# Kernel optimization log

Measured on AMD Instinct MI355X. Metric: run time of the kernel, lower is better.

Reference implementation:

```python
import jax, jax.numpy as jnp
import numpy as np

B, T, H = 2, 2048, 1024
DFF = 4 * H        # dense_mlp hidden width
E = 8              # num_experts_temp
TOP_K = 2


def setup_inputs() -> dict:
    key = jax.random.key(0)
    ks = jax.random.split(key, 6)
    s_h = 1.0 / np.sqrt(H)
    s_f = 1.0 / np.sqrt(DFF)
    return {
        "hidden_states": jax.random.normal(ks[0], (B, T, H), dtype=jnp.float32),
        "router_w": jax.random.normal(ks[1], (E, H), dtype=jnp.float32) * s_h,
        "w1": jax.random.normal(ks[2], (E, H, DFF), dtype=jnp.float32) * s_h,
        "b1": jnp.zeros((E, DFF), dtype=jnp.float32),
        "w2": jax.random.normal(ks[3], (E, DFF, H), dtype=jnp.float32) * s_f,
        "b2": jnp.zeros((E, H), dtype=jnp.float32),
    }


def reference(hidden_states, router_w, w1, b1, w2, b2):
    # Router: [B,T,E]
    router_logits = jnp.einsum("bth,eh->bte", hidden_states, router_w)
    topk_vals, topk_idx = jax.lax.top_k(router_logits, TOP_K)        # [B,T,K]
    topk_w = jax.nn.softmax(topk_vals.astype(jnp.float32), axis=-1)
    topk_w = topk_w.astype(hidden_states.dtype)

    # Dense compute of ALL experts (faithful to the original module).
    h = jnp.einsum("bth,ehf->btef", hidden_states, w1) + b1          # [B,T,E,DFF]
    h = jax.nn.gelu(h)
    expert_out = jnp.einsum("btef,efh->bteh", h, w2) + b2            # [B,T,E,H]

    # Gather top-k experts per token and mix.
    topk_out = jnp.take_along_axis(expert_out, topk_idx[..., None], axis=2)  # [B,T,K,H]
    mixed = jnp.sum(topk_out * topk_w[..., None], axis=2)            # [B,T,H]
    return mixed
```

## Files before the change

### kernel.cpp

```cpp
#include <hip/hip_runtime.h>
#include <hip/hip_bf16.h>
#include <stdint.h>

#define AS1 __attribute__((address_space(1)))
#define AS3 __attribute__((address_space(3)))

typedef __bf16 bf16x8 __attribute__((ext_vector_type(8)));
typedef float floatx4 __attribute__((ext_vector_type(4)));

static constexpr int NTOK = 4096;
static constexpr int H    = 1024;
static constexpr int DFF  = 4096;
static constexpr int E    = 8;
static constexpr int BM   = 128;
static constexpr int BN   = 128;
static constexpr int MAXROWS = 9216;

static constexpr size_t OFF_WS    = 0;
static constexpr size_t OFF_XCS   = 67108864;
static constexpr size_t OFF_HS    = 85983232;
static constexpr size_t OFF_RTIDX = 161480704;
static constexpr size_t OFF_RTW   = 161513472;
static constexpr size_t OFF_PTOK  = 161546240;
static constexpr size_t OFF_PW    = 161583104;
static constexpr size_t OFF_CNT   = 161619968;
static constexpr size_t WS_NEED   = 161620068;

__device__ __forceinline__ unsigned short f2bf(float f) {
    __bf16 b = (__bf16)f;
    return __builtin_bit_cast(unsigned short, b);
}

__device__ __forceinline__ void gload16(const void* g, void* l) {
    __builtin_amdgcn_global_load_lds((AS1 void*)g, (AS3 void*)l, 16, 0, 0);
}

__global__ __launch_bounds__(256) void k_router(const float* __restrict__ x,
                                                const float* __restrict__ rw,
                                                int* __restrict__ rt_idx,
                                                float* __restrict__ rt_w,
                                                int* __restrict__ counts) {
    const int wv = threadIdx.x >> 6, ln = threadIdx.x & 63;
    const int t = blockIdx.x * 4 + wv;
    const float* xr = x + (size_t)t * H + ln * 4;
    float4 xv[4];
#pragma unroll
    for (int c = 0; c < 4; ++c) xv[c] = *(const float4*)(xr + c * 256);
    float lg[E];
#pragma unroll
    for (int e = 0; e < E; ++e) {
        const float* rr = rw + (size_t)e * H + ln * 4;
        float acc = 0.f;
#pragma unroll
        for (int c = 0; c < 4; ++c) {
            float4 rv = *(const float4*)(rr + c * 256);
            acc += xv[c].x * rv.x + xv[c].y * rv.y + xv[c].z * rv.z + xv[c].w * rv.w;
        }
#pragma unroll
        for (int s = 32; s > 0; s >>= 1) acc += __shfl_xor(acc, s, 64);
        lg[e] = acc;
    }
    if (ln == 0) {
        int i0 = 0; float v0 = lg[0];
#pragma unroll
        for (int e = 1; e < E; ++e) if (lg[e] > v0) { v0 = lg[e]; i0 = e; }
        int i1 = -1; float v1 = -INFINITY;
#pragma unroll
        for (int e = 0; e < E; ++e) if (e != i0 && lg[e] > v1) { v1 = lg[e]; i1 = e; }
        float e1 = expf(v1 - v0);
        float inv = 1.f / (1.f + e1);
        rt_idx[2 * t] = i0; rt_idx[2 * t + 1] = i1;
        rt_w[2 * t] = inv;  rt_w[2 * t + 1] = e1 * inv;
        atomicAdd(&counts[i0], 1);
        atomicAdd(&counts[i1], 1);
    }
}

__global__ void k_offsets(const int* __restrict__ counts, int* __restrict__ offs) {
    if (threadIdx.x == 0) {
        int o = 0;
        for (int e = 0; e < E; ++e) { offs[e] = o; o += (counts[e] + BM - 1) & ~(BM - 1); }
        offs[E] = o;
    }
}

__global__ __launch_bounds__(256) void k_scatter(const int* __restrict__ rt_idx,
                                                 const float* __restrict__ rt_w,
                                                 const int* __restrict__ offs,
                                                 int* __restrict__ cursors,
                                                 int* __restrict__ pair_tok,
                                                 float* __restrict__ pair_w) {
    int t = blockIdx.x * 256 + threadIdx.x;
    if (t >= NTOK) return;
    for (int k = 0; k < 2; ++k) {
        int e = rt_idx[2 * t + k];
        int p = atomicAdd(&cursors[e], 1);
        int pos = offs[e] + p;
        pair_tok[pos] = t;
        pair_w[pos] = rt_w[2 * t + k];
    }
}

__global__ __launch_bounds__(256) void k_gather(const float* __restrict__ x,
                                                const int* __restrict__ offs,
                                                const int* __restrict__ counts,
                                                const int* __restrict__ pair_tok,
                                                unsigned short* __restrict__ xcs) {
    int pos = blockIdx.x;
    if (pos >= offs[E]) return;
    int e = 0;
    while (e < E - 1 && pos >= offs[e + 1]) ++e;
    bool valid = (pos - offs[e]) < counts[e];
    int tok = valid ? pair_tok[pos] : 0;
    int k0 = threadIdx.x * 4;
    float4 xv = valid ? *(const float4*)(x + (size_t)tok * H + k0)
                      : make_float4(0.f, 0.f, 0.f, 0.f);
    ushort4 o;
    o.x = f2bf(xv.x); o.y = f2bf(xv.y); o.z = f2bf(xv.z); o.w = f2bf(xv.w);
    int rb = pos >> 7, m = pos & 127;
    size_t idx = (((size_t)(rb * 32 + (k0 >> 5)) * 128 + m) * 32) + (((k0 >> 3) & 3) << 3) + (k0 & 7);
    *(ushort4*)(xcs + idx) = o;
}

template <int K, int N>
__global__ __launch_bounds__(256) void k_convert(const float* __restrict__ w,
                                                 unsigned short* __restrict__ ws) {
    constexpr int KB = K / 32, NB = N / 64;
    int bid = blockIdx.x;
    int nb = bid % NB, kb = (bid / NB) % KB, e = bid / (NB * KB);
    int kq = threadIdx.x & 3, nl = threadIdx.x >> 2;
    int n = nb * 64 + nl;
    const float* src = w + ((size_t)e * K + kb * 32 + kq * 8) * N + n;
    union { unsigned short us[8]; uint4 v; } u;
#pragma unroll
    for (int j = 0; j < 8; ++j) u.us[j] = f2bf(src[(size_t)j * N]);
    size_t oct = ((size_t)(e * KB + kb) * N + n) * 4 + kq;
    *(uint4*)(ws + oct * 8) = u.v;
}

template <int KTOT, int NTOT, bool IS_GEMM1, int KSPLIT>
__global__ __launch_bounds__(256) void k_gemm(const unsigned short* __restrict__ Asrc,
                                              const unsigned short* __restrict__ Bsrc,
                                              const int* __restrict__ counts,
                                              const int* __restrict__ offs,
                                              const float* __restrict__ bias,
                                              const int* __restrict__ pair_tok,
                                              const float* __restrict__ pair_w,
                                              unsigned short* __restrict__ Hs,
                                              float* __restrict__ out) {
    constexpr int KB  = KTOT / 32;
    constexpr int KBS = KB / KSPLIT;
    constexpr int MP  = 36;
    constexpr int SMEM_SHORTS = IS_GEMM1 ? (4 * 128 * MP) : 8192;

    const int e = blockIdx.y >> 5, rt = blockIdx.y & 31;
    const int cnt = counts[e];
    if (rt * BM >= cnt) return;
    const int ks = blockIdx.z;
    const int off = offs[e];
    const int rb = (off >> 7) + rt;
    const int n0 = blockIdx.x * BN;

    __shared__ unsigned short smem[SMEM_SHORTS];
    unsigned short* lds_a = smem;
    unsigned short* lds_b = smem + 4096;

    const int tid = threadIdx.x;
    const int wv = tid >> 6, ln = tid & 63;
    const int quad = ln >> 4, lr = ln & 15;
    const int wm = (wv & 1) * 64, wn = (wv >> 1) * 64;

    floatx4 acc[4][4];
#pragma unroll
    for (int i = 0; i < 4; ++i)
#pragma unroll
        for (int j = 0; j < 4; ++j) acc[i][j] = (floatx4){0.f, 0.f, 0.f, 0.f};

    const unsigned short* Atile = Asrc + (size_t)rb * KB * 4096;
    const unsigned short* Btile = Bsrc + ((size_t)e * KB * NTOT + n0) * 32;

    for (int kb = ks * KBS; kb < ks * KBS + KBS; ++kb) {
        __syncthreads();
        const unsigned short* a_src = Atile + (size_t)kb * 4096 + (wv * 2) * 512 + ln * 8;
        const unsigned short* b_src = Btile + (size_t)kb * NTOT * 32 + (wv * 2) * 512 + ln * 8;
#pragma unroll
        for (int c = 0; c < 2; ++c) {
            gload16(a_src + c * 512, &lds_a[(wv * 2 + c) * 512]);
            gload16(b_src + c * 512, &lds_b[(wv * 2 + c) * 512]);
        }
        __syncthreads();
        bf16x8 af[4], bg[4];
#pragma unroll
        for (int i = 0; i < 4; ++i) {
            af[i] = *(const bf16x8*)(lds_a + (wm + i * 16 + lr) * 32 + quad * 8);
            bg[i] = *(const bf16x8*)(lds_b + (wn + i * 16 + lr) * 32 + quad * 8);
        }
#pragma unroll
        for (int i = 0; i < 4; ++i)
#pragma unroll
            for (int j = 0; j < 4; ++j)
                acc[i][j] = __builtin_amdgcn_mfma_f32_16x16x32_bf16(af[i], bg[j], acc[i][j], 0, 0, 0);
    }

    if (IS_GEMM1) {
        float bj[4];
#pragma unroll
        for (int j = 0; j < 4; ++j) bj[j] = bias[(size_t)e * NTOT + n0 + wn + j * 16 + lr];
        __syncthreads();
#pragma unroll
        for (int j = 0; j < 4; ++j) {
            const int fl = wn + j * 16 + lr;
            const int fb = fl >> 5, f5 = fl & 31;
            unsigned short* dst = smem + fb * (128 * MP) + f5;
#pragma unroll
            for (int i = 0; i < 4; ++i) {
#pragma unroll
                for (int r = 0; r < 4; ++r) {
                    const int m = wm + i * 16 + quad * 4 + r;
                    float v = acc[i][j][r] + bj[j];
                    float u = 0.79788456080286535588f * (v + 0.044715f * v * v * v);
                    float ez = __expf(2.f * u);
                    float g = v * (1.f - 1.f / (ez + 1.f));
                    dst[m * MP] = f2bf(g);
                }
            }
        }
        __syncthreads();
        const size_t hsbase = ((size_t)rb * 128 + (n0 >> 5)) * 4096;
#pragma unroll
        for (int it = 0; it < 8; ++it) {
            const int g = (it * 256 + tid) * 8;
            const int fb = g >> 12, rem = g & 4095, m = rem >> 5, f5 = rem & 31;
            const unsigned short* s = smem + fb * (128 * MP) + m * MP + f5;
            uint2 lo = *(const uint2*)s;
            uint2 hi = *(const uint2*)(s + 4);
            uint4 v4 = make_uint4(lo.x, lo.y, hi.x, hi.y);
            *(uint4*)(Hs + hsbase + (size_t)g) = v4;
        }
    } else {
        float bj[4];
#pragma unroll
        for (int j = 0; j < 4; ++j)
            bj[j] = (ks == 0) ? bias[(size_t)e * NTOT + n0 + wn + j * 16 + lr] : 0.f;
#pragma unroll
        for (int i = 0; i < 4; ++i) {
#pragma unroll
            for (int r = 0; r < 4; ++r) {
                const int m = wm + i * 16 + quad * 4 + r;
                const int lm = rt * BM + m;
                if (lm < cnt) {
                    const int pos = off + lm;
                    const int tok = pair_tok[pos];
                    const float wgt = pair_w[pos];
#pragma unroll
                    for (int j = 0; j < 4; ++j) {
                        const int n = n0 + wn + j * 16 + lr;
                        unsafeAtomicAdd(&out[(size_t)tok * H + n], wgt * (acc[i][j][r] + bj[j]));
                    }
                }
            }
        }
    }
}

extern "C" void kernel_launch(void* const* d_in, const int* in_sizes, int n_in,
                              void* d_out, int out_size, void* d_ws, size_t ws_size,
                              hipStream_t stream) {
    const float* x  = (const float*)d_in[0];
    const float* rw = (const float*)d_in[1];
    const float* w1 = (const float*)d_in[2];
    const float* b1 = (const float*)d_in[3];
    const float* w2 = (const float*)d_in[4];
    const float* b2 = (const float*)d_in[5];
    float* out = (float*)d_out;
    char* ws = (char*)d_ws;
    if (ws_size < WS_NEED) return;

    unsigned short* Ws   = (unsigned short*)(ws + OFF_WS);
    unsigned short* XcS  = (unsigned short*)(ws + OFF_XCS);
    unsigned short* Hs   = (unsigned short*)(ws + OFF_HS);
    int*   rt_idx   = (int*)(ws + OFF_RTIDX);
    float* rt_w     = (float*)(ws + OFF_RTW);
    int*   pair_tok = (int*)(ws + OFF_PTOK);
    float* pair_w   = (float*)(ws + OFF_PW);
    int*   cnt      = (int*)(ws + OFF_CNT);
    int*   cur      = cnt + 8;
    int*   offs     = cnt + 16;

    hipMemsetAsync(cnt, 0, 64, stream);
    hipMemsetAsync(out, 0, (size_t)out_size * 4, stream);

    k_router<<<NTOK / 4, 256, 0, stream>>>(x, rw, rt_idx, rt_w, cnt);
    k_offsets<<<1, 64, 0, stream>>>(cnt, offs);
    k_scatter<<<NTOK / 256, 256, 0, stream>>>(rt_idx, rt_w, offs, cur, pair_tok, pair_w);
    k_gather<<<MAXROWS, 256, 0, stream>>>(x, offs, cnt, pair_tok, XcS);

    k_convert<H, DFF><<<8 * (H / 32) * (DFF / 64), 256, 0, stream>>>(w1, Ws);
    k_gemm<H, DFF, true, 1><<<dim3(DFF / BN, 256, 1), 256, 0, stream>>>(
        XcS, Ws, cnt, offs, b1, pair_tok, pair_w, Hs, out);

    k_convert<DFF, H><<<8 * (DFF / 32) * (H / 64), 256, 0, stream>>>(w2, Ws);
    k_gemm<DFF, H, false, 4><<<dim3(H / BN, 256, 4), 256, 0, stream>>>(
        Hs, Ws, cnt, offs, b2, pair_tok, pair_w, Hs, out);
}
```

Baseline: 738.3 us.

## Replace atomic scatter in expert GEMM2 with split-K partials and a mix kernel

GEMM2 no longer adds weighted results into the output with float atomics. It drops split-K from 4 to 2 and writes bf16 partial tiles into two buffers, reusing the gathered-input buffer as P0. A new per-token mix kernel reads both partials for both chosen experts via a new tok_pos map and writes the output directly, so the output memset is also removed. The grid shrinks to the live row-block count, with each block finding its expert from the offsets. In exchange there is an extra launch and bf16 rounding of the partial sums.

New measurement: 689.8 us. 1.07x faster.

```diff
diff --git a/kernel.cpp b/kernel.cpp
--- a/kernel.cpp
+++ b/kernel.cpp
@@ -12,23 +12,28 @@
 static constexpr int H    = 1024;
 static constexpr int DFF  = 4096;
 static constexpr int E    = 8;
-static constexpr int BM   = 128;
 static constexpr int BN   = 128;
-static constexpr int MAXROWS = 9216;
-
-static constexpr size_t OFF_WS    = 0;
-static constexpr size_t OFF_XCS   = 67108864;
-static constexpr size_t OFF_HS    = 85983232;
-static constexpr size_t OFF_RTIDX = 161480704;
-static constexpr size_t OFF_RTW   = 161513472;
-static constexpr size_t OFF_PTOK  = 161546240;
-static constexpr size_t OFF_PW    = 161583104;
-static constexpr size_t OFF_CNT   = 161619968;
-static constexpr size_t WS_NEED   = 161620068;
+static constexpr int RBMAX = 72;
+
+static constexpr size_t OFF_WS     = 0;
+static constexpr size_t OFF_XCS    = 67108864;
+static constexpr size_t OFF_HS     = 85983232;
+static constexpr size_t OFF_P1     = 161480704;
+static constexpr size_t OFF_RTIDX  = 180355072;
+static constexpr size_t OFF_RTW    = 180387840;
+static constexpr size_t OFF_PTOK   = 180420608;
+static constexpr size_t OFF_PW     = 180457472;
+static constexpr size_t OFF_TOKPOS = 180494336;
+static constexpr size_t OFF_CNT    = 180527104;
+static constexpr size_t WS_NEED    = 180527232;
 
 __device__ __forceinline__ unsigned short f2bf(float f) {
     __bf16 b = (__bf16)f;
     return __builtin_bit_cast(unsigned short, b);
+}
+__device__ __forceinline__ float bf2f(unsigned short u) {
+    unsigned int v = ((unsigned int)u) << 16;
+    return __builtin_bit_cast(float, v);
 }
 
 __device__ __forceinline__ void gload16(const void* g, void* l) {
@@ -79,7 +84,7 @@
 __global__ void k_offsets(const int* __restrict__ counts, int* __restrict__ offs) {
     if (threadIdx.x == 0) {
         int o = 0;
-        for (int e = 0; e < E; ++e) { offs[e] = o; o += (counts[e] + BM - 1) & ~(BM - 1); }
+        for (int e = 0; e < E; ++e) { offs[e] = o; o += (counts[e] + 127) & ~127; }
         offs[E] = o;
     }
 }
@@ -89,7 +94,8 @@
                                                  const int* __restrict__ offs,
                                                  int* __restrict__ cursors,
                                                  int* __restrict__ pair_tok,
-                                                 float* __restrict__ pair_w) {
+                                                 float* __restrict__ pair_w,
+                                                 int* __restrict__ tok_pos) {
     int t = blockIdx.x * 256 + threadIdx.x;
     if (t >= NTOK) return;
     for (int k = 0; k < 2; ++k) {
@@ -98,6 +104,7 @@
         int pos = offs[e] + p;
         pair_tok[pos] = t;
         pair_w[pos] = rt_w[2 * t + k];
+        tok_pos[2 * t + k] = pos;
     }
 }
 
@@ -138,30 +145,20 @@
     *(uint4*)(ws + oct * 8) = u.v;
 }
 
-template <int KTOT, int NTOT, bool IS_GEMM1, int KSPLIT>
-__global__ __launch_bounds__(256) void k_gemm(const unsigned short* __restrict__ Asrc,
-                                              const unsigned short* __restrict__ Bsrc,
-                                              const int* __restrict__ counts,
-                                              const int* __restrict__ offs,
-                                              const float* __restrict__ bias,
-                                              const int* __restrict__ pair_tok,
-                                              const float* __restrict__ pair_w,
-                                              unsigned short* __restrict__ Hs,
-                                              float* __restrict__ out) {
-    constexpr int KB  = KTOT / 32;
-    constexpr int KBS = KB / KSPLIT;
-    constexpr int MP  = 36;
-    constexpr int SMEM_SHORTS = IS_GEMM1 ? (4 * 128 * MP) : 8192;
-
-    const int e = blockIdx.y >> 5, rt = blockIdx.y & 31;
-    const int cnt = counts[e];
-    if (rt * BM >= cnt) return;
-    const int ks = blockIdx.z;
-    const int off = offs[e];
-    const int rb = (off >> 7) + rt;
+__global__ __launch_bounds__(256) void k_gemm1(const unsigned short* __restrict__ Xc,
+                                               const unsigned short* __restrict__ W1s,
+                                               const int* __restrict__ offs,
+                                               const float* __restrict__ b1,
+                                               unsigned short* __restrict__ Hs) {
+    constexpr int KB = H / 32;
+    constexpr int MP = 36;
+    const int rb = blockIdx.y;
+    if (rb * 128 >= offs[E]) return;
+    int e = 0;
+    while (e < E - 1 && rb * 128 >= offs[e + 1]) ++e;
     const int n0 = blockIdx.x * BN;
 
-    __shared__ unsigned short smem[SMEM_SHORTS];
+    __shared__ unsigned short smem[4 * 128 * MP];
     unsigned short* lds_a = smem;
     unsigned short* lds_b = smem + 4096;
 
@@ -176,13 +173,104 @@
 #pragma unroll
         for (int j = 0; j < 4; ++j) acc[i][j] = (floatx4){0.f, 0.f, 0.f, 0.f};
 
-    const unsigned short* Atile = Asrc + (size_t)rb * KB * 4096;
-    const unsigned short* Btile = Bsrc + ((size_t)e * KB * NTOT + n0) * 32;
+    const unsigned short* Atile = Xc + (size_t)rb * KB * 4096;
+    const unsigned short* Btile = W1s + ((size_t)e * KB * DFF + n0) * 32;
+
+    for (int kb = 0; kb < KB; ++kb) {
+        __syncthreads();
+        const unsigned short* a_src = Atile + (size_t)kb * 4096 + (wv * 2) * 512 + ln * 8;
+        const unsigned short* b_src = Btile + (size_t)kb * DFF * 32 + (wv * 2) * 512 + ln * 8;
+#pragma unroll
+        for (int c = 0; c < 2; ++c) {
+            gload16(a_src + c * 512, &lds_a[(wv * 2 + c) * 512]);
+            gload16(b_src + c * 512, &lds_b[(wv * 2 + c) * 512]);
+        }
+        __syncthreads();
+        bf16x8 af[4], bg[4];
+#pragma unroll
+        for (int i = 0; i < 4; ++i) {
+            af[i] = *(const bf16x8*)(lds_a + (wm + i * 16 + lr) * 32 + quad * 8);
+            bg[i] = *(const bf16x8*)(lds_b + (wn + i * 16 + lr) * 32 + quad * 8);
+        }
+#pragma unroll
+        for (int i = 0; i < 4; ++i)
+#pragma unroll
+            for (int j = 0; j < 4; ++j)
+                acc[i][j] = __builtin_amdgcn_mfma_f32_16x16x32_bf16(af[i], bg[j], acc[i][j], 0, 0, 0);
+    }
+
+    float bj[4];
+#pragma unroll
+    for (int j = 0; j < 4; ++j) bj[j] = b1[(size_t)e * DFF + n0 + wn + j * 16 + lr];
+    __syncthreads();
+#pragma unroll
+    for (int j = 0; j < 4; ++j) {
+        const int fl = wn + j * 16 + lr;
+        const int fb = fl >> 5, f5 = fl & 31;
+        unsigned short* dst = smem + fb * (128 * MP) + f5;
+#pragma unroll
+        for (int i = 0; i < 4; ++i) {
+#pragma unroll
+            for (int r = 0; r < 4; ++r) {
+                const int m = wm + i * 16 + quad * 4 + r;
+                float v = acc[i][j][r] + bj[j];
+                float u = 0.79788456080286535588f * (v + 0.044715f * v * v * v);
+                float ez = __expf(2.f * u);
+                float g = v * (1.f - 1.f / (ez + 1.f));
+                dst[m * MP] = f2bf(g);
+            }
+        }
+    }
+    __syncthreads();
+    const size_t hsbase = ((size_t)rb * 128 + (n0 >> 5)) * 4096;
+#pragma unroll
+    for (int it = 0; it < 8; ++it) {
+        const int g = (it * 256 + tid) * 8;
+        const int fb = g >> 12, rem = g & 4095, m = rem >> 5, f5 = rem & 31;
+        const unsigned short* s = smem + fb * (128 * MP) + m * MP + f5;
+        uint2 lo = *(const uint2*)s;
+        uint2 hi = *(const uint2*)(s + 4);
+        *(uint4*)(Hs + hsbase + (size_t)g) = make_uint4(lo.x, lo.y, hi.x, hi.y);
+    }
+}
+
+__global__ __launch_bounds__(256) void k_gemm2(const unsigned short* __restrict__ Hs,
+                                               const unsigned short* __restrict__ W2s,
+                                               const int* __restrict__ offs,
+                                               const float* __restrict__ b2,
+                                               unsigned short* __restrict__ P0,
+                                               unsigned short* __restrict__ P1) {
+    constexpr int KB = DFF / 32;
+    constexpr int KBS = KB / 2;
+    const int rb = blockIdx.y;
+    if (rb * 128 >= offs[E]) return;
+    int e = 0;
+    while (e < E - 1 && rb * 128 >= offs[e + 1]) ++e;
+    const int ks = blockIdx.z;
+    const int n0 = blockIdx.x * BN;
+
+    __shared__ unsigned short smem[8192];
+    unsigned short* lds_a = smem;
+    unsigned short* lds_b = smem + 4096;
+
+    const int tid = threadIdx.x;
+    const int wv = tid >> 6, ln = tid & 63;
+    const int quad = ln >> 4, lr = ln & 15;
+    const int wm = (wv & 1) * 64, wn = (wv >> 1) * 64;
+
+    floatx4 acc[4][4];
+#pragma unroll
+    for (int i = 0; i < 4; ++i)
+#pragma unroll
+        for (int j = 0; j < 4; ++j) acc[i][j] = (floatx4){0.f, 0.f, 0.f, 0.f};
+
+    const unsigned short* Atile = Hs + (size_t)rb * KB * 4096;
+    const unsigned short* Btile = W2s + ((size_t)e * KB * H + n0) * 32;
 
     for (int kb = ks * KBS; kb < ks * KBS + KBS; ++kb) {
         __syncthreads();
         const unsigned short* a_src = Atile + (size_t)kb * 4096 + (wv * 2) * 512 + ln * 8;
-        const unsigned short* b_src = Btile + (size_t)kb * NTOT * 32 + (wv * 2) * 512 + ln * 8;
+        const unsigned short* b_src = Btile + (size_t)kb * H * 32 + (wv * 2) * 512 + ln * 8;
 #pragma unroll
         for (int c = 0; c < 2; ++c) {
             gload16(a_src + c * 512, &lds_a[(wv * 2 + c) * 512]);
@@ -202,65 +290,43 @@
                 acc[i][j] = __builtin_amdgcn_mfma_f32_16x16x32_bf16(af[i], bg[j], acc[i][j], 0, 0, 0);
     }
 
-    if (IS_GEMM1) {
-        float bj[4];
-#pragma unroll
-        for (int j = 0; j < 4; ++j) bj[j] = bias[(size_t)e * NTOT + n0 + wn + j * 16 + lr];
-        __syncthreads();
-#pragma unroll
-        for (int j = 0; j < 4; ++j) {
-            const int fl = wn + j * 16 + lr;
-            const int fb = fl >> 5, f5 = fl & 31;
-            unsigned short* dst = smem + fb * (128 * MP) + f5;
-#pragma unroll
-            for (int i = 0; i < 4; ++i) {
-#pragma unroll
-                for (int r = 0; r < 4; ++r) {
-                    const int m = wm + i * 16 + quad * 4 + r;
-                    float v = acc[i][j][r] + bj[j];
-                    float u = 0.79788456080286535588f * (v + 0.044715f * v * v * v);
-                    float ez = __expf(2.f * u);
-                    float g = v * (1.f - 1.f / (ez + 1.f));
-                    dst[m * MP] = f2bf(g);
-                }
-            }
-        }
-        __syncthreads();
-        const size_t hsbase = ((size_t)rb * 128 + (n0 >> 5)) * 4096;
-#pragma unroll
-        for (int it = 0; it < 8; ++it) {
-            const int g = (it * 256 + tid) * 8;
-            const int fb = g >> 12, rem = g & 4095, m = rem >> 5, f5 = rem & 31;
-            const unsigned short* s = smem + fb * (128 * MP) + m * MP + f5;
-            uint2 lo = *(const uint2*)s;
-            uint2 hi = *(const uint2*)(s + 4);
-            uint4 v4 = make_uint4(lo.x, lo.y, hi.x, hi.y);
-            *(uint4*)(Hs + hsbase + (size_t)g) = v4;
-        }
-    } else {
-        float bj[4];
-#pragma unroll
-        for (int j = 0; j < 4; ++j)
-            bj[j] = (ks == 0) ? bias[(size_t)e * NTOT + n0 + wn + j * 16 + lr] : 0.f;
-#pragma unroll
-        for (int i = 0; i < 4; ++i) {
-#pragma unroll
-            for (int r = 0; r < 4; ++r) {
-                const int m = wm + i * 16 + quad * 4 + r;
-                const int lm = rt * BM + m;
-                if (lm < cnt) {
-                    const int pos = off + lm;
-                    const int tok = pair_tok[pos];
-                    const float wgt = pair_w[pos];
-#pragma unroll
-                    for (int j = 0; j < 4; ++j) {
-                        const int n = n0 + wn + j * 16 + lr;
-                        unsafeAtomicAdd(&out[(size_t)tok * H + n], wgt * (acc[i][j][r] + bj[j]));
-                    }
-                }
-            }
-        }
-    }
+    float bj[4];
+#pragma unroll
+    for (int j = 0; j < 4; ++j)
+        bj[j] = (ks == 0) ? b2[(size_t)e * H + n0 + wn + j * 16 + lr] : 0.f;
+    unsigned short* P = ks ? P1 : P0;
+#pragma unroll
+    for (int i = 0; i < 4; ++i) {
+#pragma unroll
+        for (int r = 0; r < 4; ++r) {
+            const int m = wm + i * 16 + quad * 4 + r;
+            unsigned short* row = P + (size_t)(rb * 128 + m) * H + n0;
+#pragma unroll
+            for (int j = 0; j < 4; ++j)
+                row[wn + j * 16 + lr] = f2bf(acc[i][j][r] + bj[j]);
+        }
+    }
+}
+
+__global__ __launch_bounds__(256) void k_mix(const unsigned short* __restrict__ P0,
+                                             const unsigned short* __restrict__ P1,
+                                             const int* __restrict__ tok_pos,
+                                             const float* __restrict__ rt_w,
+                                             float* __restrict__ out) {
+    const int t = blockIdx.x;
+    const int c = threadIdx.x * 4;
+    const int p0 = tok_pos[2 * t], p1 = tok_pos[2 * t + 1];
+    const float w0 = rt_w[2 * t], w1 = rt_w[2 * t + 1];
+    ushort4 a0 = *(const ushort4*)(P0 + (size_t)p0 * H + c);
+    ushort4 a1 = *(const ushort4*)(P1 + (size_t)p0 * H + c);
+    ushort4 b0 = *(const ushort4*)(P0 + (size_t)p1 * H + c);
+    ushort4 b1 = *(const ushort4*)(P1 + (size_t)p1 * H + c);
+    float4 o;
+    o.x = w0 * (bf2f(a0.x) + bf2f(a1.x)) + w1 * (bf2f(b0.x) + bf2f(b1.x));
+    o.y = w0 * (bf2f(a0.y) + bf2f(a1.y)) + w1 * (bf2f(b0.y) + bf2f(b1.y));
+    o.z = w0 * (bf2f(a0.z) + bf2f(a1.z)) + w1 * (bf2f(b0.z) + bf2f(b1.z));
+    o.w = w0 * (bf2f(a0.w) + bf2f(a1.w)) + w1 * (bf2f(b0.w) + bf2f(b1.w));
+    *(float4*)(out + (size_t)t * H + c) = o;
 }
 
 extern "C" void kernel_launch(void* const* d_in, const int* in_sizes, int n_in,
@@ -279,27 +345,28 @@
     unsigned short* Ws   = (unsigned short*)(ws + OFF_WS);
     unsigned short* XcS  = (unsigned short*)(ws + OFF_XCS);
     unsigned short* Hs   = (unsigned short*)(ws + OFF_HS);
+    unsigned short* P1   = (unsigned short*)(ws + OFF_P1);
     int*   rt_idx   = (int*)(ws + OFF_RTIDX);
     float* rt_w     = (float*)(ws + OFF_RTW);
     int*   pair_tok = (int*)(ws + OFF_PTOK);
     float* pair_w   = (float*)(ws + OFF_PW);
+    int*   tok_pos  = (int*)(ws + OFF_TOKPOS);
     int*   cnt      = (int*)(ws + OFF_CNT);
     int*   cur      = cnt + 8;
     int*   offs     = cnt + 16;
 
-    hipMemsetAsync(cnt, 0, 64, stream);
-    hipMemsetAsync(out, 0, (size_t)out_size * 4, stream);
+    hipMemsetAsync(cnt, 0, 128, stream);
 
     k_router<<<NTOK / 4, 256, 0, stream>>>(x, rw, rt_idx, rt_w, cnt);
     k_offsets<<<1, 64, 0, stream>>>(cnt, offs);
-    k_scatter<<<NTOK / 256, 256, 0, stream>>>(rt_idx, rt_w, offs, cur, pair_tok, pair_w);
-    k_gather<<<MAXROWS, 256, 0, stream>>>(x, offs, cnt, pair_tok, XcS);
+    k_scatter<<<NTOK / 256, 256, 0, stream>>>(rt_idx, rt_w, offs, cur, pair_tok, pair_w, tok_pos);
+    k_gather<<<9216, 256, 0, stream>>>(x, offs, cnt, pair_tok, XcS);
 
     k_convert<H, DFF><<<8 * (H / 32) * (DFF / 64), 256, 0, stream>>>(w1, Ws);
-    k_gemm<H, DFF, true, 1><<<dim3(DFF / BN, 256, 1), 256, 0, stream>>>(
-        XcS, Ws, cnt, offs, b1, pair_tok, pair_w, Hs, out);
+    k_gemm1<<<dim3(DFF / BN, RBMAX), 256, 0, stream>>>(XcS, Ws, offs, b1, Hs);
 
     k_convert<DFF, H><<<8 * (DFF / 32) * (H / 64), 256, 0, stream>>>(w2, Ws);
-    k_gemm<DFF, H, false, 4><<<dim3(H / BN, 256, 4), 256, 0, stream>>>(
-        Hs, Ws, cnt, offs, b2, pair_tok, pair_w, Hs, out);
-}
+    k_gemm2<<<dim3(H / BN, RBMAX, 2), 256, 0, stream>>>(Hs, Ws, offs, b2, XcS, P1);
+
+    k_mix<<<NTOK, 256, 0, stream>>>(XcS, P1, tok_pos, rt_w, out);
+}
```
